# Optimization experiments

Measured on AMD Instinct MI355X. Metric: run time of the kernel, lower is better.

## Reference

```python
import jax, jax.numpy as jnp
import numpy as np

# Irreps config: input/output = 32x0e + 16x1o (dim 80), H=4 heads -> head = 8x0e + 4x1o (dim 20)
M0, M1 = 32, 16      # input muls for 0e / 1o
m0, m1 = 8, 4        # per-head muls
H = 4
HEAD_DIM = m0 + 3 * m1   # 20
WNUM = H * (M0 * m0 + M1 * m0 + M0 * m1 + M1 * m1)  # 2304 per-edge TP weights
NB, HID = 16, 64
SQRT3 = np.float32(np.sqrt(3.0))
EPS = 1e-8


def radial_mlp(x, W1, b1, W2, b2):
    return jax.nn.silu(x @ W1 + b1) @ W2 + b2


def tp_edge(ss, vv, sh0, sh1, w):
    """FullyConnectedTensorProduct (32x0e+16x1o) x (1x0e+1x1o) -> H*(8x0e+4x1o) with per-edge weights w [E, WNUM].
    Paths: 0e*0e->0e, 1o*1o->0e (CG dot/sqrt3), 0e*1o->1o, 1o*0e->1o; path norm 1/sqrt(fan_in)."""
    E = ss.shape[0]
    per = M0 * m0 + M1 * m0 + M0 * m1 + M1 * m1  # 576
    w = w.reshape(E, H, per)
    o = 0
    Wss = w[..., o:o + M0 * m0].reshape(E, H, M0, m0); o += M0 * m0
    Wvv = w[..., o:o + M1 * m0].reshape(E, H, M1, m0); o += M1 * m0
    Wsv = w[..., o:o + M0 * m1].reshape(E, H, M0, m1); o += M0 * m1
    Wvs = w[..., o:o + M1 * m1].reshape(E, H, M1, m1)
    fan = np.float32(np.sqrt(M0 + M1))  # fan_in = 48 for both output irreps
    vv_dot = jnp.einsum('eui,ei->eu', vv, sh1) / SQRT3
    out0 = (jnp.einsum('eu,ehuw->ehw', ss * sh0[:, None], Wss)
            + jnp.einsum('eu,ehuw->ehw', vv_dot, Wvv)) / fan          # [E,H,m0]
    out1 = (jnp.einsum('eu,ehuw->ehw', ss, Wsv)[..., None] * sh1[:, None, None, :]
            + jnp.einsum('eui,ehuw->ehwi', vv * sh0[:, None, None], Wvs)) / fan  # [E,H,m1,3]
    return out0, out1


def setup_inputs() -> dict:
    key = jax.random.key(0)
    ks = jax.random.split(key, 24)
    N, E = 2000, 32000
    g = lambda k, s, sc=1.0: jax.random.normal(k, s, jnp.float32) * sc
    inp = {}
    inp['node_features'] = g(ks[0], (N, M0 + 3 * M1))
    inp['edge_index'] = jax.random.randint(ks[1], (2, E), 0, N)
    inp['edge_sh'] = g(ks[2], (E, 4))
    inp['edge_radial_emb'] = jax.random.uniform(ks[3], (E, NB), jnp.float32)
    # query e3nn Linear (per-head blocks)
    inp['Wq0'] = g(ks[4], (H, M0, m0))
    inp['Wq1'] = g(ks[5], (H, M1, m1))
    # radial MLPs for key / value TP weights
    inp['Wk1'] = g(ks[6], (NB, HID), 1 / np.sqrt(NB)); inp['bk1'] = jnp.zeros((HID,), jnp.float32)
    inp['Wk2'] = g(ks[7], (HID, WNUM), 1 / np.sqrt(HID)); inp['bk2'] = jnp.zeros((WNUM,), jnp.float32)
    inp['Wv1'] = g(ks[8], (NB, HID), 1 / np.sqrt(NB)); inp['bv1'] = jnp.zeros((HID,), jnp.float32)
    inp['Wv2'] = g(ks[9], (HID, WNUM), 1 / np.sqrt(HID)); inp['bv2'] = jnp.zeros((WNUM,), jnp.float32)
    # single-head dot-product TP -> 0e (shared weights)
    inp['Wd0'] = g(ks[10], (m0, m0))
    inp['Wd1'] = g(ks[11], (m1, m1))
    # output projection Linear (all heads mixed per irrep)
    inp['Wo0'] = g(ks[12], (H * m0, M0))
    inp['Wo1'] = g(ks[13], (H * m1, M1))
    # FFN: out irreps -> (2*M0)x0e + M1x1o -> out irreps
    inp['Wf1_0'] = g(ks[14], (M0, 2 * M0))
    inp['Wf1_1'] = g(ks[15], (M1, M1))
    inp['Wf2_0'] = g(ks[16], (2 * M0, M0))
    inp['Wf2_1'] = g(ks[17], (M1, M1))
    return inp


def reference(node_features, edge_index, edge_sh, edge_radial_emb,
              Wq0, Wq1, Wk1, bk1, Wk2, bk2, Wv1, bv1, Wv2, bv2,
              Wd0, Wd1, Wo0, Wo1, Wf1_0, Wf1_1, Wf2_0, Wf2_1):
    N = node_features.shape[0]
    s = node_features[:, :M0]                       # [N, M0] scalars
    v = node_features[:, M0:].reshape(N, M1, 3)     # [N, M1, 3] vectors
    src, dst = edge_index[0], edge_index[1]

    # query Linear (e3nn: per-irrep channel mix, norm 1/sqrt(fan_in))
    q0 = jnp.einsum('nu,huw->nhw', s, Wq0) / np.sqrt(M0)
    q1 = jnp.einsum('nui,huw->nhwi', v, Wq1) / np.sqrt(M1)

    sh0, sh1 = edge_sh[:, 0], edge_sh[:, 1:4]
    ss, vv = s[src], v[src]                         # gather per edge

    wk = radial_mlp(edge_radial_emb, Wk1, bk1, Wk2, bk2)
    wv = radial_mlp(edge_radial_emb, Wv1, bv1, Wv2, bv2)
    k0, k1 = tp_edge(ss, vv, sh0, sh1, wk)
    v0, v1 = tp_edge(ss, vv, sh0, sh1, wv)

    # per-head equivariant dot product -> 0e logits
    qd0, qd1 = q0[dst], q1[dst]
    fan_d = np.float32(np.sqrt(m0 * m0 + m1 * m1))
    logits = (jnp.einsum('ehu,uv,ehv->eh', qd0, Wd0, k0)
              + jnp.einsum('ehui,uv,ehvi->eh', qd1, Wd1, k1) / SQRT3) / fan_d
    logits = logits / np.sqrt(HEAD_DIM)             # self.scale
    logits = jnp.clip(logits, -10.0, 10.0)

    # scatter softmax over edges sharing a destination node
    seg_max = jax.ops.segment_max(logits, dst, num_segments=N)
    seg_max = jnp.maximum(seg_max, -10.0)           # handle empty segments
    ex = jnp.exp(logits - seg_max[dst])
    denom = jax.ops.segment_sum(ex, dst, num_segments=N)
    alpha = ex / (denom[dst] + 1e-12)               # [E, H]

    agg0 = jax.ops.segment_sum(alpha[..., None] * v0, dst, num_segments=N)        # [N,H,m0]
    agg1 = jax.ops.segment_sum(alpha[..., None, None] * v1, dst, num_segments=N)  # [N,H,m1,3]

    # output projection Linear over concatenated heads
    o0 = agg0.reshape(N, H * m0) @ Wo0 / np.sqrt(H * m0)
    o1 = jnp.einsum('nui,uw->nwi', agg1.reshape(N, H * m1, 3), Wo1) / np.sqrt(H * m1)

    # residual (input irreps == output irreps -> identity skip)
    x0 = s + o0
    x1 = v + o1

    # FFN with SafeNormActivation
    f0 = x0 @ Wf1_0 / np.sqrt(M0)                               # [N, 2*M0]
    f1 = jnp.einsum('nui,uw->nwi', x1, Wf1_1) / np.sqrt(M1)     # [N, M1, 3]
    a0 = jax.nn.silu(f0)
    norms = jnp.linalg.norm(f1, axis=-1, keepdims=True)
    safe = jnp.maximum(norms, EPS)
    a1 = jnp.where(norms < EPS, 0.0, (f1 / safe) * jax.nn.silu(norms))
    g0 = a0 @ Wf2_0 / np.sqrt(2 * M0)
    g1 = jnp.einsum('nui,uw->nwi', a1, Wf2_1) / np.sqrt(M1)

    out0 = x0 + g0
    out1 = x1 + g1
    return jnp.concatenate([out0, out1.reshape(N, M1 * 3)], axis=-1)
```

## Files before the change

kernel.cpp:

```cpp
#include <hip/hip_runtime.h>

typedef unsigned int uint;
typedef unsigned short ushort;
typedef __attribute__((ext_vector_type(8))) short bf16x8;
typedef __attribute__((ext_vector_type(4))) float f32x4;

#define N_NODES 2000
#define N_EDGES 32000
#define WNUM 2304

constexpr size_t OFF_AGG0 = 0;
constexpr size_t OFF_AGG1 = 64000;
constexpr size_t OFF_DEN  = 160000;
constexpr size_t OFF_CNT  = 168000;
constexpr size_t OFF_FLAG = 170000;
constexpr size_t OFF_W2T  = 170004;
constexpr size_t OFF_QT0  = 317460;
constexpr size_t OFF_QT1  = 381460;
constexpr size_t OFF_EORD = 477460;

__device__ __forceinline__ float b2f(ushort u){ union{uint i; float f;}x; x.i=((uint)u)<<16; return x.f; }
__device__ __forceinline__ float lo16(uint w){ union{uint u; float f;}x; x.u=w<<16; return x.f; }
__device__ __forceinline__ float hi16(uint w){ union{uint u; float f;}x; x.u=w&0xFFFF0000u; return x.f; }
__device__ __forceinline__ ushort f2b(float f){
  union{float f; uint u;}x; x.f=f;
  uint r = (x.u + 0x7FFFu + ((x.u>>16)&1u)) >> 16;
  return (ushort)r;
}
__device__ __forceinline__ float siluf(float x){ return x / (1.f + __expf(-x)); }

template<bool F32>
__device__ __forceinline__ float ldf(const void* p, int i){
  if (F32) return ((const float*)p)[i];
  return b2f(((const ushort*)p)[i]);
}
__device__ __forceinline__ float ldfr(const void* p, int i, bool f32){
  return f32 ? ((const float*)p)[i] : b2f(((const ushort*)p)[i]);
}

template<bool F32>
__device__ void prep_body(
    const void* __restrict__ nf, const int* __restrict__ eidx,
    const void* __restrict__ Wk2, const void* __restrict__ Wv2,
    const void* __restrict__ Wq0, const void* __restrict__ Wq1,
    const void* __restrict__ Wd0, const void* __restrict__ Wd1,
    ushort* __restrict__ W2T, float* __restrict__ qt0, float* __restrict__ qt1,
    int* __restrict__ cnt){
  const int t = threadIdx.x;
  const int bid = blockIdx.x;

  if (bid < 72){
    __shared__ ushort tile[64][66];
    const int mat = bid / 36, jt = bid - mat*36;
    const void* W = mat ? Wv2 : Wk2;
    const int j0 = jt*64;
    const int jo = t & 63, cb = t >> 6;
    #pragma unroll
    for (int k=0; k<16; ++k){
      const int c = cb + k*4;
      tile[c][jo] = F32 ? f2b(((const float*)W)[(size_t)c*WNUM + j0 + jo])
                        : ((const ushort*)W)[(size_t)c*WNUM + j0 + jo];
    }
    __syncthreads();
    const int jl = t >> 2, c0 = (t & 3)*16;
    ushort* dst = W2T + (size_t)mat*147456 + (size_t)(j0+jl)*64 + c0;
    #pragma unroll
    for (int k=0; k<16; ++k) dst[k] = tile[c0+k][jl];
  } else if (bid < 104){
    __shared__ float nfL[64][80];
    __shared__ float wq0L[1024], wq1L[256], wd0L[64], wd1L[16];
    const int nb = bid - 72, n0 = nb*64;
    for (int idx=t; idx<64*80; idx+=256){
      const int nn = n0 + idx/80;
      nfL[idx/80][idx%80] = (nn < N_NODES) ? ldf<F32>(nf, nn*80 + idx%80) : 0.f;
    }
    for (int idx=t; idx<1024; idx+=256) wq0L[idx] = ldf<F32>(Wq0, idx);
    if (t < 256) wq1L[t] = ldf<F32>(Wq1, t);
    if (t < 64)  wd0L[t] = ldf<F32>(Wd0, t);
    if (t < 16)  wd1L[t] = ldf<F32>(Wd1, t);
    __syncthreads();
    const int nl = t >> 2, h = t & 3;
    const int nn = n0 + nl;
    if (nn < N_NODES){
      const float* S = &nfL[nl][0];
      float q0[8];
      #pragma unroll
      for (int w=0; w<8; ++w){
        float a = 0.f;
        #pragma unroll
        for (int u=0; u<32; ++u) a += S[u]*wq0L[h*256 + u*8 + w];
        q0[w] = a * 0.17677669529663687f;
      }
      #pragma unroll
      for (int vv=0; vv<8; ++vv){
        float a = 0.f;
        #pragma unroll
        for (int u=0; u<8; ++u) a += q0[u]*wd0L[u*8+vv];
        qt0[nn*32 + h*8 + vv] = a;
      }
      float q1[12];
      #pragma unroll
      for (int w=0; w<4; ++w)
        #pragma unroll
        for (int i=0; i<3; ++i){
          float a = 0.f;
          #pragma unroll
          for (int u=0; u<16; ++u) a += S[32+u*3+i]*wq1L[h*64 + u*4 + w];
          q1[w*3+i] = a * 0.25f;
        }
      #pragma unroll
      for (int vv=0; vv<4; ++vv)
        #pragma unroll
        for (int i=0; i<3; ++i){
          float a = 0.f;
          #pragma unroll
          for (int u=0; u<4; ++u) a += q1[u*3+i]*wd1L[u*4+vv];
          qt1[nn*48 + h*12 + vv*3 + i] = a;
        }
    }
  } else {
    const int e = (bid-104)*256 + t;
    if (e < N_EDGES) atomicAdd(cnt + eidx[N_EDGES + e], 1);
  }
}

__global__ __launch_bounds__(256) void prep_kernel(
    const void* nf, const int* eidx,
    const void* Wk2, const void* Wv2,
    const void* Wq0, const void* Wq1,
    const void* Wd0, const void* Wd1,
    ushort* W2T, float* qt0, float* qt1,
    int* cnt, int* flag){
  __shared__ int s_cnt;
  const int t = threadIdx.x;
  if (t == 0) s_cnt = 0;
  __syncthreads();
  {
    uint u = ((const ushort*)nf)[t*2];
    uint ex = (u >> 7) & 0xFFu;
    if (ex >= 0xA0u) atomicAdd(&s_cnt, 1);
  }
  __syncthreads();
  const bool F32 = (s_cnt >= 20);
  if (blockIdx.x == 0 && t == 0) *flag = F32 ? 1 : 0;
  if (F32) prep_body<true >(nf, eidx, Wk2, Wv2, Wq0, Wq1, Wd0, Wd1, W2T, qt0, qt1, cnt);
  else     prep_body<false>(nf, eidx, Wk2, Wv2, Wq0, Wq1, Wd0, Wd1, W2T, qt0, qt1, cnt);
}

__global__ __launch_bounds__(256) void scan_kernel(int* __restrict__ cnt){
  __shared__ int ls[256];
  const int t = threadIdx.x;
  const int base = t*8;
  int v[8]; int s = 0;
  #pragma unroll
  for (int k=0; k<8; ++k){ int idx = base+k; v[k] = (idx < N_NODES) ? cnt[idx] : 0; s += v[k]; }
  ls[t] = s; __syncthreads();
  for (int off=1; off<256; off<<=1){
    int x = (t >= off) ? ls[t-off] : 0;
    __syncthreads();
    ls[t] += x;
    __syncthreads();
  }
  int ex = ls[t] - s;
  #pragma unroll
  for (int k=0; k<8; ++k){ int idx = base+k; if (idx < N_NODES){ int c = v[k]; cnt[idx] = ex; ex += c; } }
}

__global__ __launch_bounds__(256) void scat_kernel(const int* __restrict__ eidx,
                                                   int* __restrict__ cnt, int* __restrict__ eord){
  int e = blockIdx.x*256 + threadIdx.x;
  if (e < N_EDGES){
    int p = atomicAdd(cnt + eidx[N_EDGES + e], 1);
    eord[p] = e;
  }
}

struct Smem {
  ushort hidA[2][32][72];
  float fssT[32][36];
  float fvvT[16][36];
  float sslT[32][36];
  float vshT[16][3][36];
  float sh1T[3][36];
  float cont[4][32][21];
  int   dstL[32];
};

template<bool F32>
__device__ void edge_body(
    const void* __restrict__ nf,  const int* __restrict__ eidx,
    const int* __restrict__ eord,
    const void* __restrict__ esh, const void* __restrict__ emb,
    const void* __restrict__ Wk1, const void* __restrict__ bk1, const void* __restrict__ bk2,
    const void* __restrict__ Wv1, const void* __restrict__ bv1, const void* __restrict__ bv2,
    const ushort* __restrict__ W2T,
    const float* __restrict__ qt0g, const float* __restrict__ qt1g,
    float* __restrict__ agg0, float* __restrict__ agg1, float* __restrict__ denom,
    Smem& sm){
  const int t  = threadIdx.x;
  const int hw = t >> 5;
  const int r  = t & 31;
  const int geb = blockIdx.x*32;

  #pragma unroll 1
  for (int e=0; e<4; ++e){
    const int le = hw*4+e;
    const int ge = eord[geb+le];
    const int src = eidx[ge], d = eidx[N_EDGES+ge];
    const float sh0 = ldf<F32>(esh, ge*4+0);
    const float s1a = ldf<F32>(esh, ge*4+1), s1b = ldf<F32>(esh, ge*4+2), s1c = ldf<F32>(esh, ge*4+3);
    if (r == 0) sm.dstL[le] = d;
    if (r < 3) sm.sh1T[r][le] = (r==0)? s1a : (r==1)? s1b : s1c;
    float sv = ldf<F32>(nf, src*80 + r);
    sm.sslT[r][le] = sv;
    sm.fssT[r][le] = sv * sh0;
    if (r < 16){
      float v0 = ldf<F32>(nf, src*80+32+r*3+0);
      float v1 = ldf<F32>(nf, src*80+32+r*3+1);
      float v2 = ldf<F32>(nf, src*80+32+r*3+2);
      sm.vshT[r][0][le] = v0*sh0; sm.vshT[r][1][le] = v1*sh0; sm.vshT[r][2][le] = v2*sh0;
      sm.fvvT[r][le] = (v0*s1a + v1*s1b + v2*s1c) * 0.5773502691896258f;
    }
  }

  #pragma unroll 1
  for (int e=0; e<4; ++e){
    const int le = hw*4+e;
    const int ge = eord[geb+le];
    float em[16];
    if (F32){
      const float4* p = (const float4*)((const float*)emb + ge*16);
      float4 a=p[0], b=p[1], c=p[2], d4=p[3];
      em[0]=a.x; em[1]=a.y; em[2]=a.z; em[3]=a.w;
      em[4]=b.x; em[5]=b.y; em[6]=b.z; em[7]=b.w;
      em[8]=c.x; em[9]=c.y; em[10]=c.z; em[11]=c.w;
      em[12]=d4.x; em[13]=d4.y; em[14]=d4.z; em[15]=d4.w;
    } else {
      const uint4* p = (const uint4*)((const ushort*)emb + ge*16);
      uint4 a=p[0], b=p[1];
      em[0]=lo16(a.x); em[1]=hi16(a.x); em[2]=lo16(a.y); em[3]=hi16(a.y);
      em[4]=lo16(a.z); em[5]=hi16(a.z); em[6]=lo16(a.w); em[7]=hi16(a.w);
      em[8]=lo16(b.x); em[9]=hi16(b.x); em[10]=lo16(b.y); em[11]=hi16(b.y);
      em[12]=lo16(b.z); em[13]=hi16(b.z); em[14]=lo16(b.w); em[15]=hi16(b.w);
    }
    #pragma unroll
    for (int cc=0; cc<2; ++cc){
      const int c = r + cc*32;
      float ak = ldf<F32>(bk1, c), av = ldf<F32>(bv1, c);
      #pragma unroll
      for (int b=0; b<16; ++b){
        ak += em[b] * ldf<F32>(Wk1, b*64 + c);
        av += em[b] * ldf<F32>(Wv1, b*64 + c);
      }
      sm.hidA[0][le][c] = f2b(siluf(ak));
      sm.hidA[1][le][c] = f2b(siluf(av));
    }
  }
  __syncthreads();

  const int h = t >> 6;
  const int lane = t & 63, q = lane >> 4, n = lane & 15;
  const ushort* w2tk = W2T;
  const ushort* w2tv = W2T + 147456;

  bf16x8 af[2][2][2];
  #pragma unroll
  for (int kv=0; kv<2; ++kv)
    #pragma unroll
    for (int Mt=0; Mt<2; ++Mt)
      #pragma unroll
      for (int kh=0; kh<2; ++kh)
        af[kv][Mt][kh] = *(const bf16x8*)&sm.hidA[kv][Mt*16+n][kh*32 + q*8];

  float aK0[2][4], aV0[2][4], aPK[2][4], aPV[2][4], aWK[3][2][4], aWV[3][2][4];
  #pragma unroll
  for (int Mt=0; Mt<2; ++Mt)
    #pragma unroll
    for (int z=0; z<4; ++z){
      aK0[Mt][z]=0.f; aV0[Mt][z]=0.f; aPK[Mt][z]=0.f; aPV[Mt][z]=0.f;
      aWK[0][Mt][z]=0.f; aWK[1][Mt][z]=0.f; aWK[2][Mt][z]=0.f;
      aWV[0][Mt][z]=0.f; aWV[1][Mt][z]=0.f; aWV[2][Mt][z]=0.f;
    }

  #pragma unroll 2
  for (int tl=0; tl<24; ++tl){
    const size_t tb = ((size_t)((h*36+tl)*16 + n))*64 + q*8;
    bf16x8 bk0 = *(const bf16x8*)(w2tk + tb), bk1f = *(const bf16x8*)(w2tk + tb + 32);
    bf16x8 bv0 = *(const bf16x8*)(w2tv + tb), bv1f = *(const bf16x8*)(w2tv + tb + 32);
    const int j = h*576 + tl*16 + n;
    const float bbk = ldf<F32>(bk2, j), bbv = ldf<F32>(bv2, j);
    const bool ss = (tl < 16);
    const int u = ss ? (tl*2 + (n>>3)) : ((tl-16)*2 + (n>>3));
    #pragma unroll
    for (int Mt=0; Mt<2; ++Mt){
      f32x4 fv = ss ? *(const f32x4*)&sm.fssT[u][Mt*16+q*4]
                    : *(const f32x4*)&sm.fvvT[u][Mt*16+q*4];
      f32x4 ck = {bbk,bbk,bbk,bbk};
      ck = __builtin_amdgcn_mfma_f32_16x16x32_bf16(af[0][Mt][0], bk0, ck, 0,0,0);
      ck = __builtin_amdgcn_mfma_f32_16x16x32_bf16(af[0][Mt][1], bk1f, ck, 0,0,0);
      f32x4 cv = {bbv,bbv,bbv,bbv};
      cv = __builtin_amdgcn_mfma_f32_16x16x32_bf16(af[1][Mt][0], bv0, cv, 0,0,0);
      cv = __builtin_amdgcn_mfma_f32_16x16x32_bf16(af[1][Mt][1], bv1f, cv, 0,0,0);
      #pragma unroll
      for (int z=0; z<4; ++z){ aK0[Mt][z] += ck[z]*fv[z]; aV0[Mt][z] += cv[z]*fv[z]; }
    }
  }
  #pragma unroll 2
  for (int tl=24; tl<32; ++tl){
    const size_t tb = ((size_t)((h*36+tl)*16 + n))*64 + q*8;
    bf16x8 bk0 = *(const bf16x8*)(w2tk + tb), bk1f = *(const bf16x8*)(w2tk + tb + 32);
    bf16x8 bv0 = *(const bf16x8*)(w2tv + tb), bv1f = *(const bf16x8*)(w2tv + tb + 32);
    const int j = h*576 + tl*16 + n;
    const float bbk = ldf<F32>(bk2, j), bbv = ldf<F32>(bv2, j);
    const int u = (tl-24)*4 + (n>>2);
    #pragma unroll
    for (int Mt=0; Mt<2; ++Mt){
      f32x4 fv = *(const f32x4*)&sm.sslT[u][Mt*16+q*4];
      f32x4 ck = {bbk,bbk,bbk,bbk};
      ck = __builtin_amdgcn_mfma_f32_16x16x32_bf16(af[0][Mt][0], bk0, ck, 0,0,0);
      ck = __builtin_amdgcn_mfma_f32_16x16x32_bf16(af[0][Mt][1], bk1f, ck, 0,0,0);
      f32x4 cv = {bbv,bbv,bbv,bbv};
      cv = __builtin_amdgcn_mfma_f32_16x16x32_bf16(af[1][Mt][0], bv0, cv, 0,0,0);
      cv = __builtin_amdgcn_mfma_f32_16x16x32_bf16(af[1][Mt][1], bv1f, cv, 0,0,0);
      #pragma unroll
      for (int z=0; z<4; ++z){ aPK[Mt][z] += ck[z]*fv[z]; aPV[Mt][z] += cv[z]*fv[z]; }
    }
  }
  #pragma unroll 1
  for (int tl=32; tl<36; ++tl){
    const size_t tb = ((size_t)((h*36+tl)*16 + n))*64 + q*8;
    bf16x8 bk0 = *(const bf16x8*)(w2tk + tb), bk1f = *(const bf16x8*)(w2tk + tb + 32);
    bf16x8 bv0 = *(const bf16x8*)(w2tv + tb), bv1f = *(const bf16x8*)(w2tv + tb + 32);
    const int j = h*576 + tl*16 + n;
    const float bbk = ldf<F32>(bk2, j), bbv = ldf<F32>(bv2, j);
    const int u = (tl-32)*4 + (n>>2);
    #pragma unroll
    for (int Mt=0; Mt<2; ++Mt){
      f32x4 ck = {bbk,bbk,bbk,bbk};
      ck = __builtin_amdgcn_mfma_f32_16x16x32_bf16(af[0][Mt][0], bk0, ck, 0,0,0);
      ck = __builtin_amdgcn_mfma_f32_16x16x32_bf16(af[0][Mt][1], bk1f, ck, 0,0,0);
      f32x4 cv = {bbv,bbv,bbv,bbv};
      cv = __builtin_amdgcn_mfma_f32_16x16x32_bf16(af[1][Mt][0], bv0, cv, 0,0,0);
      cv = __builtin_amdgcn_mfma_f32_16x16x32_bf16(af[1][Mt][1], bv1f, cv, 0,0,0);
      #pragma unroll
      for (int i=0; i<3; ++i){
        f32x4 fv = *(const f32x4*)&sm.vshT[u][i][Mt*16+q*4];
        #pragma unroll
        for (int z=0; z<4; ++z){ aWK[i][Mt][z] += ck[z]*fv[z]; aWV[i][Mt][z] += cv[z]*fv[z]; }
      }
    }
  }

  #pragma unroll
  for (int Mt=0; Mt<2; ++Mt)
    #pragma unroll
    for (int z=0; z<4; ++z){
      aK0[Mt][z] += __shfl_xor(aK0[Mt][z], 8, 64);
      aV0[Mt][z] += __shfl_xor(aV0[Mt][z], 8, 64);
      aPK[Mt][z] += __shfl_xor(aPK[Mt][z], 4, 64);
      aPK[Mt][z] += __shfl_xor(aPK[Mt][z], 8, 64);
      aPV[Mt][z] += __shfl_xor(aPV[Mt][z], 4, 64);
      aPV[Mt][z] += __shfl_xor(aPV[Mt][z], 8, 64);
      #pragma unroll
      for (int i=0; i<3; ++i){
        aWK[i][Mt][z] += __shfl_xor(aWK[i][Mt][z], 4, 64);
        aWK[i][Mt][z] += __shfl_xor(aWK[i][Mt][z], 8, 64);
        aWV[i][Mt][z] += __shfl_xor(aWV[i][Mt][z], 4, 64);
        aWV[i][Mt][z] += __shfl_xor(aWV[i][Mt][z], 8, 64);
      }
    }

  const float invfan = 0.14433756729740643f;
  int dn[2][4];
  #pragma unroll
  for (int Mt=0; Mt<2; ++Mt)
    #pragma unroll
    for (int z=0; z<4; ++z) dn[Mt][z] = sm.dstL[Mt*16 + q*4 + z];

  f32x4 s1v[3][2];
  #pragma unroll
  for (int i=0; i<3; ++i)
    #pragma unroll
    for (int Mt=0; Mt<2; ++Mt)
      s1v[i][Mt] = *(const f32x4*)&sm.sh1T[i][Mt*16+q*4];

  float lgp[2][4];
  #pragma unroll
  for (int Mt=0; Mt<2; ++Mt)
    #pragma unroll
    for (int z=0; z<4; ++z){
      float acc = 0.f;
      if (n < 8) acc = qt0g[dn[Mt][z]*32 + h*8 + n] * aK0[Mt][z];
      if (n < 4){
        float s = 0.f;
        #pragma unroll
        for (int i=0; i<3; ++i){
          float k1 = aPK[Mt][z]*s1v[i][Mt][z] + aWK[i][Mt][z];
          s += qt1g[dn[Mt][z]*48 + h*12 + n*3 + i] * k1;
        }
        acc += s * 0.5773502691896258f;
      }
      lgp[Mt][z] = acc;
    }
  #pragma unroll
  for (int Mt=0; Mt<2; ++Mt)
    #pragma unroll
    for (int z=0; z<4; ++z){
      lgp[Mt][z] += __shfl_xor(lgp[Mt][z], 1, 64);
      lgp[Mt][z] += __shfl_xor(lgp[Mt][z], 2, 64);
      lgp[Mt][z] += __shfl_xor(lgp[Mt][z], 4, 64);
      lgp[Mt][z] += __shfl_xor(lgp[Mt][z], 8, 64);
    }

  #pragma unroll
  for (int Mt=0; Mt<2; ++Mt)
    #pragma unroll
    for (int z=0; z<4; ++z){
      float lg = lgp[Mt][z] * invfan * 0.025f;
      lg = fminf(10.f, fmaxf(-10.f, lg));
      const float ex = __expf(lg - 10.0f);
      const int el = Mt*16 + q*4 + z;
      if (n == 0) sm.cont[h][el][0] = ex;
      if (n < 8)  sm.cont[h][el][1+n] = ex * aV0[Mt][z] * invfan;
      if (n < 4){
        #pragma unroll
        for (int i=0; i<3; ++i){
          float v1 = (aPV[Mt][z]*s1v[i][Mt][z] + aWV[i][Mt][z]) * invfan;
          sm.cont[h][el][9+n*3+i] = ex * v1;
        }
      }
    }
  __syncthreads();

  if (t < 84){
    const int h2 = t / 21, comp = t - h2*21;
    float acc = 0.f;
    #pragma unroll 1
    for (int e2=0; e2<32; ++e2){
      acc += sm.cont[h2][e2][comp];
      const int d2 = sm.dstL[e2];
      if (e2 == 31 || sm.dstL[e2+1] != d2){
        if (comp == 0)      atomicAdd(denom + d2*4  + h2, acc);
        else if (comp < 9)  atomicAdd(agg0  + d2*32 + h2*8  + (comp-1), acc);
        else                atomicAdd(agg1  + d2*48 + h2*12 + (comp-9), acc);
        acc = 0.f;
      }
    }
  }
}

__global__ __launch_bounds__(256) void edge_kernel(
    const void* nf, const int* eidx, const int* eord, const void* esh, const void* emb,
    const void* Wk1, const void* bk1, const void* bk2,
    const void* Wv1, const void* bv1, const void* bv2,
    const ushort* W2T, const float* qt0g, const float* qt1g,
    float* agg0, float* agg1, float* denom, const int* flag){
  __shared__ Smem sm;
  if (*flag)
    edge_body<true >(nf,eidx,eord,esh,emb,Wk1,bk1,bk2,Wv1,bv1,bv2,W2T,qt0g,qt1g,agg0,agg1,denom,sm);
  else
    edge_body<false>(nf,eidx,eord,esh,emb,Wk1,bk1,bk2,Wv1,bv1,bv2,W2T,qt0g,qt1g,agg0,agg1,denom,sm);
}

__global__ __launch_bounds__(64) void node_out_kernel(
    const void* __restrict__ nf, const float* __restrict__ agg0r, const float* __restrict__ agg1r,
    const float* __restrict__ denom,
    const void* __restrict__ Wo0, const void* __restrict__ Wo1,
    const void* __restrict__ Wf10, const void* __restrict__ Wf11,
    const void* __restrict__ Wf20, const void* __restrict__ Wf21,
    void* __restrict__ out, const int* __restrict__ flag){
  __shared__ float ag0[32], ag1[48], adiv[4];
  __shared__ float x0s[32], x1s[48], a0s[64], f1s[48], coefs[16];
  const bool F32 = (*flag) != 0;
  const int n = blockIdx.x, t = threadIdx.x;
  if (t < 4) adiv[t] = 1.f / (denom[n*4+t] + 1e-12f);
  __syncthreads();
  if (t < 32) ag0[t] = agg0r[n*32+t] * adiv[t>>3];
  if (t < 48) ag1[t] = agg1r[n*48+t] * adiv[t/12];
  __syncthreads();
  if (t < 32){
    float o = 0.f;
    #pragma unroll
    for (int k=0; k<32; ++k) o += ag0[k]*ldfr(Wo0, k*32+t, F32);
    x0s[t] = ldfr(nf, n*80+t, F32) + o*0.17677669529663687f;
  }
  if (t < 48){
    int w = t/3, i = t - w*3;
    float o = 0.f;
    #pragma unroll
    for (int u=0; u<16; ++u) o += ag1[u*3+i]*ldfr(Wo1, u*16+w, F32);
    x1s[t] = ldfr(nf, n*80+32+t, F32) + o*0.25f;
  }
  __syncthreads();
  {
    float f0 = 0.f;
    #pragma unroll
    for (int u=0; u<32; ++u) f0 += x0s[u]*ldfr(Wf10, u*64+t, F32);
    a0s[t] = siluf(f0*0.17677669529663687f);
  }
  if (t < 48){
    int w = t/3, i = t - w*3;
    float f1 = 0.f;
    #pragma unroll
    for (int u=0; u<16; ++u) f1 += x1s[u*3+i]*ldfr(Wf11, u*16+w, F32);
    f1s[t] = f1*0.25f;
  }
  __syncthreads();
  if (t < 16){
    float a = f1s[t*3], b = f1s[t*3+1], c = f1s[t*3+2];
    float nrm = sqrtf(a*a+b*b+c*c);
    float safe = fmaxf(nrm, 1e-8f);
    coefs[t] = (nrm < 1e-8f) ? 0.f : siluf(nrm)/safe;
  }
  __syncthreads();
  if (t < 32){
    float g = 0.f;
    #pragma unroll
    for (int u=0; u<64; ++u) g += a0s[u]*ldfr(Wf20, u*32+t, F32);
    float val = x0s[t] + g*0.125f;
    if (F32) ((float*)out)[n*80+t] = val; else ((ushort*)out)[n*80+t] = f2b(val);
  }
  if (t < 48){
    int w = t/3, i = t - w*3;
    float g = 0.f;
    #pragma unroll
    for (int u=0; u<16; ++u) g += coefs[u]*f1s[u*3+i]*ldfr(Wf21, u*16+w, F32);
    float val = x1s[t] + g*0.25f;
    if (F32) ((float*)out)[n*80+32+t] = val; else ((ushort*)out)[n*80+32+t] = f2b(val);
  }
}

extern "C" void kernel_launch(void* const* d_in, const int* in_sizes, int n_in,
                              void* d_out, int out_size, void* d_ws, size_t ws_size,
                              hipStream_t stream){
  const void* nf   = d_in[0];
  const int*  eidx = (const int*)d_in[1];
  const void* esh  = d_in[2];
  const void* emb  = d_in[3];
  const void* Wq0  = d_in[4];
  const void* Wq1  = d_in[5];
  const void* Wk1  = d_in[6];
  const void* bk1  = d_in[7];
  const void* Wk2  = d_in[8];
  const void* bk2  = d_in[9];
  const void* Wv1  = d_in[10];
  const void* bv1  = d_in[11];
  const void* Wv2  = d_in[12];
  const void* bv2  = d_in[13];
  const void* Wd0  = d_in[14];
  const void* Wd1  = d_in[15];
  const void* Wo0  = d_in[16];
  const void* Wo1  = d_in[17];
  const void* Wf10 = d_in[18];
  const void* Wf11 = d_in[19];
  const void* Wf20 = d_in[20];
  const void* Wf21 = d_in[21];
  float* ws = (float*)d_ws;

  float* agg0  = ws + OFF_AGG0;
  float* agg1  = ws + OFF_AGG1;
  float* denom = ws + OFF_DEN;
  int*   cnt   = (int*)(ws + OFF_CNT);
  int*   flag  = (int*)(ws + OFF_FLAG);
  ushort* W2T  = (ushort*)(ws + OFF_W2T);
  float* qt0   = ws + OFF_QT0;
  float* qt1   = ws + OFF_QT1;
  int*   eord  = (int*)(ws + OFF_EORD);

  hipMemsetAsync(agg0, 0, 170000*sizeof(float), stream);
  prep_kernel<<<229, 256, 0, stream>>>(nf, eidx, Wk2, Wv2, Wq0, Wq1, Wd0, Wd1,
                                       W2T, qt0, qt1, cnt, flag);
  scan_kernel<<<1, 256, 0, stream>>>(cnt);
  scat_kernel<<<125, 256, 0, stream>>>(eidx, cnt, eord);
  edge_kernel<<<N_EDGES/32, 256, 0, stream>>>(nf, eidx, eord, esh, emb,
                                              Wk1, bk1, bk2, Wv1, bv1, bv2,
                                              W2T, qt0, qt1,
                                              agg0, agg1, denom, flag);
  node_out_kernel<<<N_NODES, 64, 0, stream>>>(nf, agg0, agg1, denom,
                                              Wo0, Wo1, Wf10, Wf11, Wf20, Wf21, d_out, flag);
}
```

Before: 239.3 us.

## Process key and value paths sequentially and alias LDS buffers to cut pressure

The edge kernel used to compute key and value tensor-product contractions together, keeping both sets of accumulators and A-fragments live at once. It now loops over key then value, reusing one set of accumulators, and stores the logits' exp in registers between the two passes. The feature staging arrays and the contribution buffer now share LDS through a union, with an added barrier before the overwrite. The aim is fewer VGPRs and less LDS per block, so more waves can be resident. The cost is less ILP between the two MFMA streams and an extra sync.

```diff
diff --git a/kernel.cpp b/kernel.cpp
--- a/kernel.cpp
+++ b/kernel.cpp
@@ -177,12 +177,16 @@
 
 struct Smem {
   ushort hidA[2][32][72];
-  float fssT[32][36];
-  float fvvT[16][36];
-  float sslT[32][36];
+  union {
+    struct {
+      float fssT[32][36];
+      float fvvT[16][36];
+      float sslT[32][36];
+    } f;
+    float cont[4][32][21];
+  } u;
   float vshT[16][3][36];
   float sh1T[3][36];
-  float cont[4][32][21];
   int   dstL[32];
 };
 
@@ -212,14 +216,14 @@
     if (r == 0) sm.dstL[le] = d;
     if (r < 3) sm.sh1T[r][le] = (r==0)? s1a : (r==1)? s1b : s1c;
     float sv = ldf<F32>(nf, src*80 + r);
-    sm.sslT[r][le] = sv;
-    sm.fssT[r][le] = sv * sh0;
+    sm.u.f.sslT[r][le] = sv;
+    sm.u.f.fssT[r][le] = sv * sh0;
     if (r < 16){
       float v0 = ldf<F32>(nf, src*80+32+r*3+0);
       float v1 = ldf<F32>(nf, src*80+32+r*3+1);
       float v2 = ldf<F32>(nf, src*80+32+r*3+2);
       sm.vshT[r][0][le] = v0*sh0; sm.vshT[r][1][le] = v1*sh0; sm.vshT[r][2][le] = v2*sh0;
-      sm.fvvT[r][le] = (v0*s1a + v1*s1b + v2*s1c) * 0.5773502691896258f;
+      sm.u.f.fvvT[r][le] = (v0*s1a + v1*s1b + v2*s1c) * 0.5773502691896258f;
     }
   }
 
@@ -260,176 +264,150 @@
 
   const int h = t >> 6;
   const int lane = t & 63, q = lane >> 4, n = lane & 15;
-  const ushort* w2tk = W2T;
-  const ushort* w2tv = W2T + 147456;
-
-  bf16x8 af[2][2][2];
-  #pragma unroll
-  for (int kv=0; kv<2; ++kv)
+  const float invfan = 0.14433756729740643f;
+  float exv[2][4];
+
+  #pragma unroll 1
+  for (int kv=0; kv<2; ++kv){
+    const ushort* wmat = W2T + (size_t)kv*147456;
+    const void* bvec = kv ? bv2 : bk2;
+    bf16x8 af[2][2];
     #pragma unroll
     for (int Mt=0; Mt<2; ++Mt)
       #pragma unroll
       for (int kh=0; kh<2; ++kh)
-        af[kv][Mt][kh] = *(const bf16x8*)&sm.hidA[kv][Mt*16+n][kh*32 + q*8];
-
-  float aK0[2][4], aV0[2][4], aPK[2][4], aPV[2][4], aWK[3][2][4], aWV[3][2][4];
-  #pragma unroll
-  for (int Mt=0; Mt<2; ++Mt)
-    #pragma unroll
-    for (int z=0; z<4; ++z){
-      aK0[Mt][z]=0.f; aV0[Mt][z]=0.f; aPK[Mt][z]=0.f; aPV[Mt][z]=0.f;
-      aWK[0][Mt][z]=0.f; aWK[1][Mt][z]=0.f; aWK[2][Mt][z]=0.f;
-      aWV[0][Mt][z]=0.f; aWV[1][Mt][z]=0.f; aWV[2][Mt][z]=0.f;
-    }
-
-  #pragma unroll 2
-  for (int tl=0; tl<24; ++tl){
-    const size_t tb = ((size_t)((h*36+tl)*16 + n))*64 + q*8;
-    bf16x8 bk0 = *(const bf16x8*)(w2tk + tb), bk1f = *(const bf16x8*)(w2tk + tb + 32);
-    bf16x8 bv0 = *(const bf16x8*)(w2tv + tb), bv1f = *(const bf16x8*)(w2tv + tb + 32);
-    const int j = h*576 + tl*16 + n;
-    const float bbk = ldf<F32>(bk2, j), bbv = ldf<F32>(bv2, j);
-    const bool ss = (tl < 16);
-    const int u = ss ? (tl*2 + (n>>3)) : ((tl-16)*2 + (n>>3));
-    #pragma unroll
-    for (int Mt=0; Mt<2; ++Mt){
-      f32x4 fv = ss ? *(const f32x4*)&sm.fssT[u][Mt*16+q*4]
-                    : *(const f32x4*)&sm.fvvT[u][Mt*16+q*4];
-      f32x4 ck = {bbk,bbk,bbk,bbk};
-      ck = __builtin_amdgcn_mfma_f32_16x16x32_bf16(af[0][Mt][0], bk0, ck, 0,0,0);
-      ck = __builtin_amdgcn_mfma_f32_16x16x32_bf16(af[0][Mt][1], bk1f, ck, 0,0,0);
-      f32x4 cv = {bbv,bbv,bbv,bbv};
-      cv = __builtin_amdgcn_mfma_f32_16x16x32_bf16(af[1][Mt][0], bv0, cv, 0,0,0);
-      cv = __builtin_amdgcn_mfma_f32_16x16x32_bf16(af[1][Mt][1], bv1f, cv, 0,0,0);
-      #pragma unroll
-      for (int z=0; z<4; ++z){ aK0[Mt][z] += ck[z]*fv[z]; aV0[Mt][z] += cv[z]*fv[z]; }
-    }
-  }
-  #pragma unroll 2
-  for (int tl=24; tl<32; ++tl){
-    const size_t tb = ((size_t)((h*36+tl)*16 + n))*64 + q*8;
-    bf16x8 bk0 = *(const bf16x8*)(w2tk + tb), bk1f = *(const bf16x8*)(w2tk + tb + 32);
-    bf16x8 bv0 = *(const bf16x8*)(w2tv + tb), bv1f = *(const bf16x8*)(w2tv + tb + 32);
-    const int j = h*576 + tl*16 + n;
-    const float bbk = ldf<F32>(bk2, j), bbv = ldf<F32>(bv2, j);
-    const int u = (tl-24)*4 + (n>>2);
-    #pragma unroll
-    for (int Mt=0; Mt<2; ++Mt){
-      f32x4 fv = *(const f32x4*)&sm.sslT[u][Mt*16+q*4];
-      f32x4 ck = {bbk,bbk,bbk,bbk};
-      ck = __builtin_amdgcn_mfma_f32_16x16x32_bf16(af[0][Mt][0], bk0, ck, 0,0,0);
-      ck = __builtin_amdgcn_mfma_f32_16x16x32_bf16(af[0][Mt][1], bk1f, ck, 0,0,0);
-      f32x4 cv = {bbv,bbv,bbv,bbv};
-      cv = __builtin_amdgcn_mfma_f32_16x16x32_bf16(af[1][Mt][0], bv0, cv, 0,0,0);
-      cv = __builtin_amdgcn_mfma_f32_16x16x32_bf16(af[1][Mt][1], bv1f, cv, 0,0,0);
-      #pragma unroll
-      for (int z=0; z<4; ++z){ aPK[Mt][z] += ck[z]*fv[z]; aPV[Mt][z] += cv[z]*fv[z]; }
-    }
-  }
-  #pragma unroll 1
-  for (int tl=32; tl<36; ++tl){
-    const size_t tb = ((size_t)((h*36+tl)*16 + n))*64 + q*8;
-    bf16x8 bk0 = *(const bf16x8*)(w2tk + tb), bk1f = *(const bf16x8*)(w2tk + tb + 32);
-    bf16x8 bv0 = *(const bf16x8*)(w2tv + tb), bv1f = *(const bf16x8*)(w2tv + tb + 32);
-    const int j = h*576 + tl*16 + n;
-    const float bbk = ldf<F32>(bk2, j), bbv = ldf<F32>(bv2, j);
-    const int u = (tl-32)*4 + (n>>2);
-    #pragma unroll
-    for (int Mt=0; Mt<2; ++Mt){
-      f32x4 ck = {bbk,bbk,bbk,bbk};
-      ck = __builtin_amdgcn_mfma_f32_16x16x32_bf16(af[0][Mt][0], bk0, ck, 0,0,0);
-      ck = __builtin_amdgcn_mfma_f32_16x16x32_bf16(af[0][Mt][1], bk1f, ck, 0,0,0);
-      f32x4 cv = {bbv,bbv,bbv,bbv};
-      cv = __builtin_amdgcn_mfma_f32_16x16x32_bf16(af[1][Mt][0], bv0, cv, 0,0,0);
-      cv = __builtin_amdgcn_mfma_f32_16x16x32_bf16(af[1][Mt][1], bv1f, cv, 0,0,0);
-      #pragma unroll
-      for (int i=0; i<3; ++i){
-        f32x4 fv = *(const f32x4*)&sm.vshT[u][i][Mt*16+q*4];
-        #pragma unroll
-        for (int z=0; z<4; ++z){ aWK[i][Mt][z] += ck[z]*fv[z]; aWV[i][Mt][z] += cv[z]*fv[z]; }
-      }
-    }
-  }
-
-  #pragma unroll
-  for (int Mt=0; Mt<2; ++Mt)
-    #pragma unroll
-    for (int z=0; z<4; ++z){
-      aK0[Mt][z] += __shfl_xor(aK0[Mt][z], 8, 64);
-      aV0[Mt][z] += __shfl_xor(aV0[Mt][z], 8, 64);
-      aPK[Mt][z] += __shfl_xor(aPK[Mt][z], 4, 64);
-      aPK[Mt][z] += __shfl_xor(aPK[Mt][z], 8, 64);
-      aPV[Mt][z] += __shfl_xor(aPV[Mt][z], 4, 64);
-      aPV[Mt][z] += __shfl_xor(aPV[Mt][z], 8, 64);
-      #pragma unroll
-      for (int i=0; i<3; ++i){
-        aWK[i][Mt][z] += __shfl_xor(aWK[i][Mt][z], 4, 64);
-        aWK[i][Mt][z] += __shfl_xor(aWK[i][Mt][z], 8, 64);
-        aWV[i][Mt][z] += __shfl_xor(aWV[i][Mt][z], 4, 64);
-        aWV[i][Mt][z] += __shfl_xor(aWV[i][Mt][z], 8, 64);
-      }
-    }
-
-  const float invfan = 0.14433756729740643f;
-  int dn[2][4];
-  #pragma unroll
-  for (int Mt=0; Mt<2; ++Mt)
-    #pragma unroll
-    for (int z=0; z<4; ++z) dn[Mt][z] = sm.dstL[Mt*16 + q*4 + z];
-
-  f32x4 s1v[3][2];
-  #pragma unroll
-  for (int i=0; i<3; ++i)
+        af[Mt][kh] = *(const bf16x8*)&sm.hidA[kv][Mt*16+n][kh*32 + q*8];
+
+    float a0[2][4], aP[2][4], aW[3][2][4];
     #pragma unroll
     for (int Mt=0; Mt<2; ++Mt)
-      s1v[i][Mt] = *(const f32x4*)&sm.sh1T[i][Mt*16+q*4];
-
-  float lgp[2][4];
-  #pragma unroll
-  for (int Mt=0; Mt<2; ++Mt)
-    #pragma unroll
-    for (int z=0; z<4; ++z){
-      float acc = 0.f;
-      if (n < 8) acc = qt0g[dn[Mt][z]*32 + h*8 + n] * aK0[Mt][z];
-      if (n < 4){
-        float s = 0.f;
+      #pragma unroll
+      for (int z=0; z<4; ++z){
+        a0[Mt][z]=0.f; aP[Mt][z]=0.f;
+        aW[0][Mt][z]=0.f; aW[1][Mt][z]=0.f; aW[2][Mt][z]=0.f;
+      }
+
+    #pragma unroll 4
+    for (int tl=0; tl<24; ++tl){
+      const size_t tb = ((size_t)((h*36+tl)*16 + n))*64 + q*8;
+      bf16x8 b0 = *(const bf16x8*)(wmat + tb), b1 = *(const bf16x8*)(wmat + tb + 32);
+      const float bb = ldf<F32>(bvec, h*576 + tl*16 + n);
+      const bool ss = (tl < 16);
+      const int u = ss ? (tl*2 + (n>>3)) : ((tl-16)*2 + (n>>3));
+      #pragma unroll
+      for (int Mt=0; Mt<2; ++Mt){
+        f32x4 fv = ss ? *(const f32x4*)&sm.u.f.fssT[u][Mt*16+q*4]
+                      : *(const f32x4*)&sm.u.f.fvvT[u][Mt*16+q*4];
+        f32x4 c = {bb,bb,bb,bb};
+        c = __builtin_amdgcn_mfma_f32_16x16x32_bf16(af[Mt][0], b0, c, 0,0,0);
+        c = __builtin_amdgcn_mfma_f32_16x16x32_bf16(af[Mt][1], b1, c, 0,0,0);
+        #pragma unroll
+        for (int z=0; z<4; ++z) a0[Mt][z] += c[z]*fv[z];
+      }
+    }
+    #pragma unroll 4
+    for (int tl=24; tl<32; ++tl){
+      const size_t tb = ((size_t)((h*36+tl)*16 + n))*64 + q*8;
+      bf16x8 b0 = *(const bf16x8*)(wmat + tb), b1 = *(const bf16x8*)(wmat + tb + 32);
+      const float bb = ldf<F32>(bvec, h*576 + tl*16 + n);
+      const int u = (tl-24)*4 + (n>>2);
+      #pragma unroll
+      for (int Mt=0; Mt<2; ++Mt){
+        f32x4 fv = *(const f32x4*)&sm.u.f.sslT[u][Mt*16+q*4];
+        f32x4 c = {bb,bb,bb,bb};
+        c = __builtin_amdgcn_mfma_f32_16x16x32_bf16(af[Mt][0], b0, c, 0,0,0);
+        c = __builtin_amdgcn_mfma_f32_16x16x32_bf16(af[Mt][1], b1, c, 0,0,0);
+        #pragma unroll
+        for (int z=0; z<4; ++z) aP[Mt][z] += c[z]*fv[z];
+      }
+    }
+    #pragma unroll
+    for (int tl=32; tl<36; ++tl){
+      const size_t tb = ((size_t)((h*36+tl)*16 + n))*64 + q*8;
+      bf16x8 b0 = *(const bf16x8*)(wmat + tb), b1 = *(const bf16x8*)(wmat + tb + 32);
+      const float bb = ldf<F32>(bvec, h*576 + tl*16 + n);
+      const int u = (tl-32)*4 + (n>>2);
+      #pragma unroll
+      for (int Mt=0; Mt<2; ++Mt){
+        f32x4 c = {bb,bb,bb,bb};
+        c = __builtin_amdgcn_mfma_f32_16x16x32_bf16(af[Mt][0], b0, c, 0,0,0);
+        c = __builtin_amdgcn_mfma_f32_16x16x32_bf16(af[Mt][1], b1, c, 0,0,0);
         #pragma unroll
         for (int i=0; i<3; ++i){
-          float k1 = aPK[Mt][z]*s1v[i][Mt][z] + aWK[i][Mt][z];
-          s += qt1g[dn[Mt][z]*48 + h*12 + n*3 + i] * k1;
-        }
-        acc += s * 0.5773502691896258f;
-      }
-      lgp[Mt][z] = acc;
-    }
-  #pragma unroll
-  for (int Mt=0; Mt<2; ++Mt)
-    #pragma unroll
-    for (int z=0; z<4; ++z){
-      lgp[Mt][z] += __shfl_xor(lgp[Mt][z], 1, 64);
-      lgp[Mt][z] += __shfl_xor(lgp[Mt][z], 2, 64);
-      lgp[Mt][z] += __shfl_xor(lgp[Mt][z], 4, 64);
-      lgp[Mt][z] += __shfl_xor(lgp[Mt][z], 8, 64);
-    }
-
-  #pragma unroll
-  for (int Mt=0; Mt<2; ++Mt)
-    #pragma unroll
-    for (int z=0; z<4; ++z){
-      float lg = lgp[Mt][z] * invfan * 0.025f;
-      lg = fminf(10.f, fmaxf(-10.f, lg));
-      const float ex = __expf(lg - 10.0f);
-      const int el = Mt*16 + q*4 + z;
-      if (n == 0) sm.cont[h][el][0] = ex;
-      if (n < 8)  sm.cont[h][el][1+n] = ex * aV0[Mt][z] * invfan;
-      if (n < 4){
+          f32x4 fv = *(const f32x4*)&sm.vshT[u][i][Mt*16+q*4];
+          #pragma unroll
+          for (int z=0; z<4; ++z) aW[i][Mt][z] += c[z]*fv[z];
+        }
+      }
+    }
+
+    #pragma unroll
+    for (int Mt=0; Mt<2; ++Mt)
+      #pragma unroll
+      for (int z=0; z<4; ++z){
+        a0[Mt][z] += __shfl_xor(a0[Mt][z], 8, 64);
+        aP[Mt][z] += __shfl_xor(aP[Mt][z], 4, 64);
+        aP[Mt][z] += __shfl_xor(aP[Mt][z], 8, 64);
         #pragma unroll
         for (int i=0; i<3; ++i){
-          float v1 = (aPV[Mt][z]*s1v[i][Mt][z] + aWV[i][Mt][z]) * invfan;
-          sm.cont[h][el][9+n*3+i] = ex * v1;
-        }
-      }
-    }
+          aW[i][Mt][z] += __shfl_xor(aW[i][Mt][z], 4, 64);
+          aW[i][Mt][z] += __shfl_xor(aW[i][Mt][z], 8, 64);
+        }
+      }
+
+    if (kv == 0){
+      float lgp[2][4];
+      #pragma unroll
+      for (int Mt=0; Mt<2; ++Mt)
+        #pragma unroll
+        for (int z=0; z<4; ++z){
+          const int el = Mt*16 + q*4 + z;
+          const int d = sm.dstL[el];
+          float acc = 0.f;
+          if (n < 8) acc = qt0g[d*32 + h*8 + n] * a0[Mt][z];
+          if (n < 4){
+            float s = 0.f;
+            #pragma unroll
+            for (int i=0; i<3; ++i){
+              float k1 = aP[Mt][z]*sm.sh1T[i][el] + aW[i][Mt][z];
+              s += qt1g[d*48 + h*12 + n*3 + i] * k1;
+            }
+            acc += s * 0.5773502691896258f;
+          }
+          lgp[Mt][z] = acc;
+        }
+      #pragma unroll
+      for (int Mt=0; Mt<2; ++Mt)
+        #pragma unroll
+        for (int z=0; z<4; ++z){
+          lgp[Mt][z] += __shfl_xor(lgp[Mt][z], 1, 64);
+          lgp[Mt][z] += __shfl_xor(lgp[Mt][z], 2, 64);
+          lgp[Mt][z] += __shfl_xor(lgp[Mt][z], 4, 64);
+          lgp[Mt][z] += __shfl_xor(lgp[Mt][z], 8, 64);
+          float lg = lgp[Mt][z] * invfan * 0.025f;
+          lg = fminf(10.f, fmaxf(-10.f, lg));
+          exv[Mt][z] = __expf(lg - 10.0f);
+        }
+    } else {
+      __syncthreads();
+      #pragma unroll
+      for (int Mt=0; Mt<2; ++Mt)
+        #pragma unroll
+        for (int z=0; z<4; ++z){
+          const int el = Mt*16 + q*4 + z;
+          const float ex = exv[Mt][z];
+          if (n == 0) sm.u.cont[h][el][0] = ex;
+          if (n < 8)  sm.u.cont[h][el][1+n] = ex * a0[Mt][z] * invfan;
+          if (n < 4){
+            #pragma unroll
+            for (int i=0; i<3; ++i){
+              float v1 = (aP[Mt][z]*sm.sh1T[i][el] + aW[i][Mt][z]) * invfan;
+              sm.u.cont[h][el][9+n*3+i] = ex * v1;
+            }
+          }
+        }
+    }
+  }
   __syncthreads();
 
   if (t < 84){
@@ -437,7 +415,7 @@
     float acc = 0.f;
     #pragma unroll 1
     for (int e2=0; e2<32; ++e2){
-      acc += sm.cont[h2][e2][comp];
+      acc += sm.u.cont[h2][e2][comp];
       const int d2 = sm.dstL[e2];
       if (e2 == 31 || sm.dstL[e2+1] != d2){
         if (comp == 0)      atomicAdd(denom + d2*4  + h2, acc);
```

New measurement: 236.4 us. About the same (-1.2%).
